# Performance work log

Measured on AMD Instinct MI355X. Metric: run time of the kernel, lower is better.

## Reference

```python
import jax, jax.numpy as jnp
import numpy as np

B, W, H, V, L = 64, 512, 1024, 32000, 2


def setup_inputs() -> dict:
    key = jax.random.key(0)
    ks = jax.random.split(key, 20)
    s = 0.02  # init scale
    n = lambda k, shp: jax.random.normal(k, shp, jnp.float32)
    return {
        "input": jax.random.randint(ks[0], (B, 1), 0, V),
        "h0": n(ks[1], (L, B, H)),
        "c0": n(ks[2], (L, B, H)),
        "encoder_output": n(ks[3], (B, W, H)),
        "embedding": n(ks[4], (V, H)) * s,
        "W_ih0": n(ks[5], (4 * H, H)) * s,
        "W_hh0": n(ks[6], (4 * H, H)) * s,
        "b_ih0": n(ks[7], (4 * H,)) * s,
        "b_hh0": n(ks[8], (4 * H,)) * s,
        "W_ih1": n(ks[9], (4 * H, H)) * s,
        "W_hh1": n(ks[10], (4 * H, H)) * s,
        "b_ih1": n(ks[11], (4 * H,)) * s,
        "b_hh1": n(ks[12], (4 * H,)) * s,
        "att_w": n(ks[13], (2 * H,)) * s,
        "att_b": n(ks[14], (1,)) * s,
        "input_W": n(ks[15], (H, 2 * H)) * s,
        "input_b": n(ks[16], (H,)) * s,
        "out_W": n(ks[17], (V, H)) * s,
        "out_b": n(ks[18], (V,)) * s,
    }


def _lstm_step(x, h, c, W_ih, W_hh, b_ih, b_hh):
    # PyTorch gate order: i, f, g, o
    g = x @ W_ih.T + h @ W_hh.T + b_ih + b_hh
    i, f, gg, o = jnp.split(g, 4, axis=-1)
    c2 = jax.nn.sigmoid(f) * c + jax.nn.sigmoid(i) * jnp.tanh(gg)
    return jax.nn.sigmoid(o) * jnp.tanh(c2), c2


def reference(input, h0, c0, encoder_output, embedding,
              W_ih0, W_hh0, b_ih0, b_hh0, W_ih1, W_hh1, b_ih1, b_hh1,
              att_w, att_b, input_W, input_b, out_W, out_b):
    Hd = h0.shape[-1]
    emb = embedding[input]                       # (B,1,H)
    att_state = h0[-1] * c0[-1]                  # (B,H)
    # Vectorized replacement of the per-word cat+linear loop:
    # att_line(cat(enc_w, att_state)) = enc_w @ w_enc + att_state @ w_st + b
    w_enc, w_st = att_w[:Hd], att_w[Hd:]
    scores = encoder_output @ w_enc + (att_state @ w_st)[:, None] + att_b[0]  # (B,W)
    # Original quirk: weigth starts with a zeros column, then softmax over
    # weigth[:, 0:-1] -> zero column + scores for words 0..W-2 (last dropped).
    zeros = jnp.zeros((scores.shape[0], 1), scores.dtype)
    full = jnp.concatenate([zeros, scores[:, :-1]], axis=1)  # (B,W)
    wts = jax.nn.softmax(full, axis=1)
    ctx = jnp.einsum('bw,bwh->bh', wts, encoder_output)      # (B,H)
    x = jnp.concatenate([ctx, emb[:, 0, :]], axis=-1)        # (B,2H)
    x = x @ input_W.T + input_b                              # (B,H)
    h1, c1 = _lstm_step(x, h0[0], c0[0], W_ih0, W_hh0, b_ih0, b_hh0)
    h2, c2 = _lstm_step(h1, h0[1], c0[1], W_ih1, W_hh1, b_ih1, b_hh1)
    logits = h2 @ out_W.T + out_b                            # (B,V)
    logp = jax.nn.log_softmax(logits, axis=-1)[:, None, :]   # (B,1,V)
    return logp, jnp.stack([h1, h2]), jnp.stack([c1, c2])
```

## Files before the change

kernel.cpp:

```cpp
#include <hip/hip_runtime.h>
#include <hip/hip_bf16.h>

#define Bsz 64
#define Wln 512
#define Hd  1024
#define Vc  32000

typedef short v8s __attribute__((ext_vector_type(8)));
typedef float f32x4 __attribute__((ext_vector_type(4)));

__device__ inline unsigned short f2b(float f) {
  union { float f; unsigned u; } v; v.f = f;
  return (unsigned short)((v.u + 0x8000u) >> 16);
}
__device__ inline float wave_sum(float v) {
  #pragma unroll
  for (int o = 32; o; o >>= 1) v += __shfl_down(v, o);
  return v;
}
__device__ inline float wave_max(float v) {
  #pragma unroll
  for (int o = 32; o; o >>= 1) v = fmaxf(v, __shfl_down(v, o));
  return v;
}
__device__ inline float wave_sum_all(float v) {
  #pragma unroll
  for (int o = 32; o; o >>= 1) v += __shfl_xor(v, o);
  return v;
}
__device__ inline float wave_max_all(float v) {
  #pragma unroll
  for (int o = 32; o; o >>= 1) v = fmaxf(v, __shfl_xor(v, o));
  return v;
}
__device__ inline float sigm(float x) { return 1.f / (1.f + expf(-x)); }

__device__ inline v8s cvt_frag(float4 x0, float4 x1) {
  v8s r;
  r[0] = (short)f2b(x0.x); r[1] = (short)f2b(x0.y);
  r[2] = (short)f2b(x0.z); r[3] = (short)f2b(x0.w);
  r[4] = (short)f2b(x1.x); r[5] = (short)f2b(x1.y);
  r[6] = (short)f2b(x1.z); r[7] = (short)f2b(x1.w);
  return r;
}

__device__ inline void stage_A(const float* __restrict__ A, const float* __restrict__ Ab,
                               int sA, char* pool, int tid) {
  #pragma unroll
  for (int it = 0; it < 16; ++it) {
    int idx = it * 512 + tid;
    int row = idx >> 7, ch = idx & 127;
    const float* src = A + (size_t)row * sA + ch * 8;
    float4 x0 = *(const float4*)src;
    float4 x1 = *(const float4*)(src + 4);
    if (Ab) {
      const float* s2 = Ab + (size_t)row * sA + ch * 8;
      float4 y0 = *(const float4*)s2;
      float4 y1 = *(const float4*)(s2 + 4);
      x0.x += y0.x; x0.y += y0.y; x0.z += y0.z; x0.w += y0.w;
      x1.x += y1.x; x1.y += y1.y; x1.z += y1.z; x1.w += y1.w;
    }
    *(v8s*)(pool + row * 2048 + ((ch * 16) ^ ((row & 7) << 4))) = cvt_frag(x0, x1);
  }
}

__global__ __launch_bounds__(512, 8) void k_attn(
    const float* __restrict__ enc, const float* __restrict__ att_w,
    const float* __restrict__ h0, const float* __restrict__ c0,
    const float* __restrict__ att_b,
    float* __restrict__ ctxp, float* __restrict__ pm_a, float* __restrict__ ps_a)
{
  __shared__ __align__(16) float pool[9 * 1024];
  __shared__ float fullv[8];
  __shared__ float redA[8];
  const int b = blockIdx.x >> 6, ch = blockIdx.x & 63;
  const int c0r = ch * 8;
  const int tid = threadIdx.x, w = tid >> 6, lane = tid & 63;
  const float* encb = enc + (size_t)b * Wln * Hd;

  #pragma unroll
  for (int it = 0; it < 5; ++it) {
    int idx = it * 512 + tid;
    if (idx < 2304) {
      int rl = idx >> 8, c4 = idx & 255;
      int gr = c0r - 1 + rl;
      gr = gr < 0 ? 0 : gr;
      float4 v = *(const float4*)(encb + (size_t)gr * Hd + c4 * 4);
      *(float4*)(pool + rl * 1024 + c4 * 4) = v;
    }
  }

  {
    size_t base = (size_t)(Bsz + b) * Hd;
    int j = tid * 2;
    float s = h0[base + j] * c0[base + j] * att_w[Hd + j]
            + h0[base + j + 1] * c0[base + j + 1] * att_w[Hd + j + 1];
    s = wave_sum(s);
    if (lane == 0) redA[w] = s;
  }
  __syncthreads();
  float sa = att_b[0];
  #pragma unroll
  for (int i = 0; i < 8; ++i) sa += redA[i];

  float4 aw[4];
  #pragma unroll
  for (int s4 = 0; s4 < 4; ++s4)
    aw[s4] = *(const float4*)(att_w + s4 * 256 + lane * 4);

  {
    int j = c0r + w;
    float v = 0.f;
    if (j > 0) {
      const float* rp = pool + w * 1024;
      float s = 0.f;
      #pragma unroll
      for (int s4 = 0; s4 < 4; ++s4) {
        float4 e = *(const float4*)(rp + s4 * 256 + lane * 4);
        s += e.x * aw[s4].x + e.y * aw[s4].y + e.z * aw[s4].z + e.w * aw[s4].w;
      }
      s = wave_sum(s);
      v = s + sa;
    }
    if (lane == 0) fullv[w] = v;
  }
  __syncthreads();

  float mv = (lane < 8) ? fullv[lane] : -1e30f;
  float M = wave_max_all(mv);
  float ev = (lane < 8) ? expf(mv - M) : 0.f;
  float S = wave_sum_all(ev);

  float wt = expf(fullv[w] - M);
  float4 a4[4];
  {
    const float* rp = pool + (w + 1) * 1024;
    #pragma unroll
    for (int s4 = 0; s4 < 4; ++s4) {
      float4 e = *(const float4*)(rp + s4 * 256 + lane * 4);
      a4[s4].x = wt * e.x; a4[s4].y = wt * e.y;
      a4[s4].z = wt * e.z; a4[s4].w = wt * e.w;
    }
  }
  __syncthreads();
  #pragma unroll
  for (int s4 = 0; s4 < 4; ++s4)
    *(float4*)(pool + w * 1024 + s4 * 256 + lane * 4) = a4[s4];
  __syncthreads();

  for (int c = tid; c < Hd; c += 512) {
    float s = 0.f;
    #pragma unroll
    for (int ww = 0; ww < 8; ++ww) s += pool[ww * 1024 + c];
    ctxp[(size_t)(b * 64 + ch) * Hd + c] = s;
  }
  if (tid == 0) { pm_a[b * 64 + ch] = M; ps_a[b * 64 + ch] = S; }
}

__global__ __launch_bounds__(512) void k_ctx_fin(
    const float* __restrict__ ctxp, const float* __restrict__ pm_a,
    const float* __restrict__ ps_a, const int* __restrict__ input,
    const float* __restrict__ emb, float* __restrict__ cat)
{
  __shared__ float scs[64];
  __shared__ float invsh;
  int b = blockIdx.x, tid = threadIdx.x;
  if (tid == 0) {
    float Mg = pm_a[b * 64];
    #pragma unroll
    for (int c = 1; c < 64; ++c) Mg = fmaxf(Mg, pm_a[b * 64 + c]);
    float Sg = 0.f;
    for (int c = 0; c < 64; ++c) {
      float e = expf(pm_a[b * 64 + c] - Mg);
      scs[c] = e;
      Sg += ps_a[b * 64 + c] * e;
    }
    invsh = 1.f / Sg;
  }
  __syncthreads();
  float inv = invsh;
  for (int h = tid; h < Hd; h += 512) {
    float s = 0.f;
    #pragma unroll 8
    for (int c = 0; c < 64; ++c) s += ctxp[(size_t)(b * 64 + c) * Hd + h] * scs[c];
    cat[b * 2 * Hd + h] = s * inv;
  }
  int idx = input[b];
  for (int j = tid; j < Hd; j += 512)
    cat[b * 2 * Hd + Hd + j] = emb[(size_t)idx * Hd + j];
}

__global__ __launch_bounds__(512) void k_input_gemm(
    const float* __restrict__ cat, const float* __restrict__ inW,
    const float* __restrict__ inb, float* __restrict__ x1, float* __restrict__ x2)
{
  __shared__ __align__(16) char pool[131072];
  const int tid = threadIdx.x;
  const int w = tid >> 6, lane = tid & 63;
  const int r = lane & 15, q = lane >> 4;
  const int kh = w;
  const int half = (blockIdx.x >= 64);
  const int n0 = (blockIdx.x & 63) * 16;
  const float* A = cat + half * 1024;
  const float* B = inW + half * 1024;
  float* out = half ? x2 : x1;

  const float* bp = B + (size_t)(n0 + r) * 2048 + kh * 128 + q * 8;
  float4 breg[4][2];
  #pragma unroll
  for (int kk = 0; kk < 4; ++kk) {
    breg[kk][0] = *(const float4*)(bp + kk * 32);
    breg[kk][1] = *(const float4*)(bp + kk * 32 + 4);
  }
  stage_A(A, nullptr, 2048, pool, tid);
  __syncthreads();

  f32x4 acc[4] = {{0,0,0,0},{0,0,0,0},{0,0,0,0},{0,0,0,0}};
  const int swz = (r & 7) << 4;
  #pragma unroll
  for (int kk = 0; kk < 4; ++kk) {
    v8s bf = cvt_frag(breg[kk][0], breg[kk][1]);
    int cb = ((kh * 128 + kk * 32 + q * 8) * 2) ^ swz;
    #pragma unroll
    for (int m = 0; m < 4; ++m) {
      v8s af = *(const v8s*)(pool + (m * 16 + r) * 2048 + cb);
      acc[m] = __builtin_amdgcn_mfma_f32_16x16x32_bf16(af, bf, acc[m], 0, 0, 0);
    }
  }
  __syncthreads();

  float (*red)[64][17] = (float(*)[64][17])pool;
  #pragma unroll
  for (int m = 0; m < 4; ++m)
    #pragma unroll
    for (int rr = 0; rr < 4; ++rr)
      red[w][lane][m * 4 + rr] = acc[m][rr];
  __syncthreads();

  #pragma unroll
  for (int it = 0; it < 2; ++it) {
    int e = it * 512 + tid;
    int cc = e & 15, rowi = e >> 4;
    int idx = ((rowi >> 4) << 2) + (rowi & 3);
    int le  = (((rowi >> 2) & 3) << 4) + cc;
    float s = 0.f;
    #pragma unroll
    for (int j = 0; j < 8; ++j) s += red[j][le][idx];
    float bb = half ? 0.f : inb[n0 + cc];
    out[(size_t)rowi * Hd + n0 + cc] = s + bb;
  }
}

__global__ __launch_bounds__(512) void k_gate_lstm(
    const float* __restrict__ xA, const float* __restrict__ xAb,
    const float* __restrict__ hA,
    const float* __restrict__ W_ih, const float* __restrict__ W_hh,
    const float* __restrict__ b_ih, const float* __restrict__ b_hh,
    const float* __restrict__ c0,
    float* __restrict__ out_h, float* __restrict__ out_c)
{
  __shared__ __align__(16) char pool[131072];
  const int tid = threadIdx.x;
  const int w = tid >> 6, lane = tid & 63;
  const int r = lane & 15, q = lane >> 4;
  const int kh = w;
  const int gate = r >> 2, jl = r & 3;
  const size_t Brow = (size_t)gate * Hd + blockIdx.x * 4 + jl;

  float4 breg[2][4][2];
  {
    const float* bp0 = W_ih + Brow * Hd + kh * 128 + q * 8;
    const float* bp1 = W_hh + Brow * Hd + kh * 128 + q * 8;
    #pragma unroll
    for (int kk = 0; kk < 4; ++kk) {
      breg[0][kk][0] = *(const float4*)(bp0 + kk * 32);
      breg[0][kk][1] = *(const float4*)(bp0 + kk * 32 + 4);
      breg[1][kk][0] = *(const float4*)(bp1 + kk * 32);
      breg[1][kk][1] = *(const float4*)(bp1 + kk * 32 + 4);
    }
  }

  f32x4 acc[4] = {{0,0,0,0},{0,0,0,0},{0,0,0,0},{0,0,0,0}};
  const float* Amat[2] = { xA, hA };
  const float* Abm[2]  = { xAb, nullptr };
  #pragma unroll
  for (int p = 0; p < 2; ++p) {
    stage_A(Amat[p], Abm[p], Hd, pool, tid);
    __syncthreads();
    const int swz = (r & 7) << 4;
    #pragma unroll
    for (int kk = 0; kk < 4; ++kk) {
      v8s bf = cvt_frag(breg[p][kk][0], breg[p][kk][1]);
      int cb = ((kh * 128 + kk * 32 + q * 8) * 2) ^ swz;
      #pragma unroll
      for (int m = 0; m < 4; ++m) {
        v8s af = *(const v8s*)(pool + (m * 16 + r) * 2048 + cb);
        acc[m] = __builtin_amdgcn_mfma_f32_16x16x32_bf16(af, bf, acc[m], 0, 0, 0);
      }
    }
    __syncthreads();
  }

  float (*red)[64][17] = (float(*)[64][17])pool;
  #pragma unroll
  for (int m = 0; m < 4; ++m)
    #pragma unroll
    for (int rr = 0; rr < 4; ++rr)
      red[w][lane][m * 4 + rr] = acc[m][rr];
  __syncthreads();

  if (tid < 256) {
    int b = tid >> 2, jl2 = tid & 3;
    int jg = blockIdx.x * 4 + jl2;
    float gv[4];
    #pragma unroll
    for (int g2 = 0; g2 < 4; ++g2) {
      int cc = g2 * 4 + jl2;
      int idx = ((b >> 4) << 2) + (b & 3);
      int le  = (((b >> 2) & 3) << 4) + cc;
      float s = 0.f;
      #pragma unroll
      for (int j = 0; j < 8; ++j) s += red[j][le][idx];
      gv[g2] = s + b_ih[(size_t)g2 * Hd + jg] + b_hh[(size_t)g2 * Hd + jg];
    }
    float c = sigm(gv[1]) * c0[(size_t)b * Hd + jg] + sigm(gv[0]) * tanhf(gv[2]);
    float h = sigm(gv[3]) * tanhf(c);
    out_h[(size_t)b * Hd + jg] = h;
    out_c[(size_t)b * Hd + jg] = c;
  }
}

__global__ __launch_bounds__(512) void k_logits(
    const float* __restrict__ A, const float* __restrict__ B,
    const float* __restrict__ bias, float* __restrict__ out,
    float* __restrict__ pm, float* __restrict__ ps)
{
  __shared__ __align__(16) char pool[131072];
  const int tid = threadIdx.x;
  const int w = tid >> 6, lane = tid & 63;
  const int r = lane & 15, q = lane >> 4;
  const int nsub = w & 3, kh = w >> 2;
  const int n0 = blockIdx.x * 64;

  const float* bp = B + (size_t)(n0 + nsub * 16 + r) * Hd + kh * 512 + q * 8;
  float4 breg[16][2];
  #pragma unroll
  for (int kk = 0; kk < 16; ++kk) {
    breg[kk][0] = *(const float4*)(bp + kk * 32);
    breg[kk][1] = *(const float4*)(bp + kk * 32 + 4);
  }
  stage_A(A, nullptr, Hd, pool, tid);
  __syncthreads();

  f32x4 acc[4] = {{0,0,0,0},{0,0,0,0},{0,0,0,0},{0,0,0,0}};
  const int swz = (r & 7) << 4;
  #pragma unroll
  for (int kk = 0; kk < 16; ++kk) {
    v8s bf = cvt_frag(breg[kk][0], breg[kk][1]);
    int cb = ((kh * 512 + kk * 32 + q * 8) * 2) ^ swz;
    #pragma unroll
    for (int m = 0; m < 4; ++m) {
      v8s af = *(const v8s*)(pool + (m * 16 + r) * 2048 + cb);
      acc[m] = __builtin_amdgcn_mfma_f32_16x16x32_bf16(af, bf, acc[m], 0, 0, 0);
    }
  }
  __syncthreads();

  float (*red)[64][17] = (float(*)[64][17])pool;
  #pragma unroll
  for (int m = 0; m < 4; ++m)
    #pragma unroll
    for (int rr = 0; rr < 4; ++rr)
      red[w][lane][m * 4 + rr] = acc[m][rr];
  __syncthreads();

  #pragma unroll
  for (int it = 0; it < 8; ++it) {
    int e = it * 512 + tid;
    int cc = e & 63, rowi = e >> 6;
    int ns2 = cc >> 4, lo = cc & 15;
    int idx = ((rowi >> 4) << 2) + (rowi & 3);
    int le  = (((rowi >> 2) & 3) << 4) + lo;
    float val = red[ns2][le][idx] + red[ns2 + 4][le][idx] + bias[n0 + cc];
    out[(size_t)rowi * Vc + n0 + cc] = val;
    float wm = wave_max_all(val);
    float we = wave_sum_all(expf(val - wm));
    if (cc == 0) { pm[blockIdx.x * 64 + rowi] = wm; ps[blockIdx.x * 64 + rowi] = we; }
  }
}

__global__ __launch_bounds__(512) void k_lsm_sub(
    float* __restrict__ lg, const float* __restrict__ pm, const float* __restrict__ ps)
{
  __shared__ float redA[8], redB[8];
  int b = blockIdx.x >> 2, qc = blockIdx.x & 3;
  int tid = threadIdx.x, w = tid >> 6, lane = tid & 63;
  float m = -1e30f;
  for (int j = tid; j < 500; j += 512) m = fmaxf(m, pm[j * 64 + b]);
  m = wave_max(m);
  if (lane == 0) redA[w] = m;
  __syncthreads();
  float M = redA[0];
  #pragma unroll
  for (int i = 1; i < 8; ++i) M = fmaxf(M, redA[i]);
  float s = 0.f;
  for (int j = tid; j < 500; j += 512) s += ps[j * 64 + b] * expf(pm[j * 64 + b] - M);
  s = wave_sum(s);
  if (lane == 0) redB[w] = s;
  __syncthreads();
  float S = redB[0];
  #pragma unroll
  for (int i = 1; i < 8; ++i) S += redB[i];
  float lse = M + logf(S);
  float* row = lg + (size_t)b * Vc + qc * 8000;
  for (int j = tid * 4; j < 8000; j += 2048) {
    float4 v = *(const float4*)(row + j);
    v.x -= lse; v.y -= lse; v.z -= lse; v.w -= lse;
    *(float4*)(row + j) = v;
  }
}

extern "C" void kernel_launch(void* const* d_in, const int* in_sizes, int n_in,
                              void* d_out, int out_size, void* d_ws, size_t ws_size,
                              hipStream_t stream)
{
  const int*   input = (const int*)d_in[0];
  const float* h0    = (const float*)d_in[1];
  const float* c0    = (const float*)d_in[2];
  const float* enc   = (const float*)d_in[3];
  const float* emb   = (const float*)d_in[4];
  const float* W_ih0 = (const float*)d_in[5];
  const float* W_hh0 = (const float*)d_in[6];
  const float* b_ih0 = (const float*)d_in[7];
  const float* b_hh0 = (const float*)d_in[8];
  const float* W_ih1 = (const float*)d_in[9];
  const float* W_hh1 = (const float*)d_in[10];
  const float* b_ih1 = (const float*)d_in[11];
  const float* b_hh1 = (const float*)d_in[12];
  const float* att_w = (const float*)d_in[13];
  const float* att_b = (const float*)d_in[14];
  const float* inW   = (const float*)d_in[15];
  const float* inb   = (const float*)d_in[16];
  const float* outW  = (const float*)d_in[17];
  const float* outb  = (const float*)d_in[18];
  float* out = (float*)d_out;

  char* ws = (char*)d_ws;
  float* cat    = (float*)(ws + 0);
  float* x1     = (float*)(ws + 524288);
  float* x2     = (float*)(ws + 786432);
  float* ctxp   = (float*)(ws + 1048576);
  float* pm_a   = (float*)(ws + 17825792);
  float* ps_a   = (float*)(ws + 17842176);
  float* pm     = (float*)(ws + 17858560);
  float* ps     = (float*)(ws + 17986560);

  float* out_h = out + (size_t)Bsz * Vc;
  float* out_c = out_h + 2 * Bsz * Hd;
  float* h1 = out_h;
  float* h2 = out_h + Bsz * Hd;

  k_attn<<<Bsz * 64, 512, 0, stream>>>(enc, att_w, h0, c0, att_b, ctxp, pm_a, ps_a);
  k_ctx_fin<<<Bsz, 512, 0, stream>>>(ctxp, pm_a, ps_a, input, emb, cat);
  k_input_gemm<<<128, 512, 0, stream>>>(cat, inW, inb, x1, x2);
  k_gate_lstm<<<256, 512, 0, stream>>>(x1, x2, h0, W_ih0, W_hh0, b_ih0, b_hh0,
                                       c0, h1, out_c);
  k_gate_lstm<<<256, 512, 0, stream>>>(h1, nullptr, h0 + (size_t)Bsz * Hd,
                                       W_ih1, W_hh1, b_ih1, b_hh1,
                                       c0 + (size_t)Bsz * Hd, h2, out_c + Bsz * Hd);
  k_logits<<<500, 512, 0, stream>>>(h2, outW, outb, out, pm, ps);
  k_lsm_sub<<<256, 512, 0, stream>>>(out, pm, ps);
}
```

Measured before the change: 149.9 us.

## Drop softmax max-tracking in attention and widen the context-finalize grid

```diff
diff --git a/kernel.cpp b/kernel.cpp
--- a/kernel.cpp
+++ b/kernel.cpp
@@ -64,30 +64,27 @@
   }
 }
 
-__global__ __launch_bounds__(512, 8) void k_attn(
+__global__ __launch_bounds__(512, 4) void k_attn(
     const float* __restrict__ enc, const float* __restrict__ att_w,
     const float* __restrict__ h0, const float* __restrict__ c0,
     const float* __restrict__ att_b,
-    float* __restrict__ ctxp, float* __restrict__ pm_a, float* __restrict__ ps_a)
-{
-  __shared__ __align__(16) float pool[9 * 1024];
-  __shared__ float fullv[8];
+    float* __restrict__ ctxp, float* __restrict__ ps_a)
+{
+  __shared__ __align__(16) float pool[8 * 1024];
+  __shared__ float dots[9];
   __shared__ float redA[8];
+  __shared__ float wts_sh[8];
   const int b = blockIdx.x >> 6, ch = blockIdx.x & 63;
   const int c0r = ch * 8;
   const int tid = threadIdx.x, w = tid >> 6, lane = tid & 63;
   const float* encb = enc + (size_t)b * Wln * Hd;
 
-  #pragma unroll
-  for (int it = 0; it < 5; ++it) {
-    int idx = it * 512 + tid;
-    if (idx < 2304) {
-      int rl = idx >> 8, c4 = idx & 255;
-      int gr = c0r - 1 + rl;
-      gr = gr < 0 ? 0 : gr;
-      float4 v = *(const float4*)(encb + (size_t)gr * Hd + c4 * 4);
-      *(float4*)(pool + rl * 1024 + c4 * 4) = v;
-    }
+  const float* rowp = encb + (size_t)(c0r + w) * Hd;
+  float4 e[4], aw[4];
+  #pragma unroll
+  for (int i = 0; i < 4; ++i) {
+    e[i]  = *(const float4*)(rowp + (i * 64 + lane) * 4);
+    aw[i] = *(const float4*)(att_w + (i * 64 + lane) * 4);
   }
 
   {
@@ -98,54 +95,41 @@
     s = wave_sum(s);
     if (lane == 0) redA[w] = s;
   }
-  __syncthreads();
+
+  {
+    float s = e[0].x*aw[0].x + e[0].y*aw[0].y + e[0].z*aw[0].z + e[0].w*aw[0].w
+            + e[1].x*aw[1].x + e[1].y*aw[1].y + e[1].z*aw[1].z + e[1].w*aw[1].w
+            + e[2].x*aw[2].x + e[2].y*aw[2].y + e[2].z*aw[2].z + e[2].w*aw[2].w
+            + e[3].x*aw[3].x + e[3].y*aw[3].y + e[3].z*aw[3].z + e[3].w*aw[3].w;
+    s = wave_sum(s);
+    if (lane == 0) dots[w + 1] = s;
+  }
+  if (w == 7 && c0r > 0) {
+    const float* hp = encb + (size_t)(c0r - 1) * Hd;
+    float s = 0.f;
+    #pragma unroll
+    for (int i = 0; i < 4; ++i) {
+      float4 hv = *(const float4*)(hp + (i * 64 + lane) * 4);
+      s += hv.x*aw[i].x + hv.y*aw[i].y + hv.z*aw[i].z + hv.w*aw[i].w;
+    }
+    s = wave_sum(s);
+    if (lane == 0) dots[0] = s;
+  }
+  __syncthreads();
+
   float sa = att_b[0];
   #pragma unroll
   for (int i = 0; i < 8; ++i) sa += redA[i];
 
-  float4 aw[4];
-  #pragma unroll
-  for (int s4 = 0; s4 < 4; ++s4)
-    aw[s4] = *(const float4*)(att_w + s4 * 256 + lane * 4);
-
-  {
-    int j = c0r + w;
-    float v = 0.f;
-    if (j > 0) {
-      const float* rp = pool + w * 1024;
-      float s = 0.f;
-      #pragma unroll
-      for (int s4 = 0; s4 < 4; ++s4) {
-        float4 e = *(const float4*)(rp + s4 * 256 + lane * 4);
-        s += e.x * aw[s4].x + e.y * aw[s4].y + e.z * aw[s4].z + e.w * aw[s4].w;
-      }
-      s = wave_sum(s);
-      v = s + sa;
-    }
-    if (lane == 0) fullv[w] = v;
-  }
-  __syncthreads();
-
-  float mv = (lane < 8) ? fullv[lane] : -1e30f;
-  float M = wave_max_all(mv);
-  float ev = (lane < 8) ? expf(mv - M) : 0.f;
-  float S = wave_sum_all(ev);
-
-  float wt = expf(fullv[w] - M);
-  float4 a4[4];
-  {
-    const float* rp = pool + (w + 1) * 1024;
-    #pragma unroll
-    for (int s4 = 0; s4 < 4; ++s4) {
-      float4 e = *(const float4*)(rp + s4 * 256 + lane * 4);
-      a4[s4].x = wt * e.x; a4[s4].y = wt * e.y;
-      a4[s4].z = wt * e.z; a4[s4].w = wt * e.w;
-    }
-  }
-  __syncthreads();
-  #pragma unroll
-  for (int s4 = 0; s4 < 4; ++s4)
-    *(float4*)(pool + w * 1024 + s4 * 256 + lane * 4) = a4[s4];
+  int rw = c0r + w;
+  float wt = (rw == 0) ? 1.f : expf(dots[w] + sa);
+  if (lane == 0) wts_sh[w] = wt;
+
+  #pragma unroll
+  for (int i = 0; i < 4; ++i) {
+    e[i].x *= wt; e[i].y *= wt; e[i].z *= wt; e[i].w *= wt;
+    *(float4*)(pool + w * 1024 + (i * 64 + lane) * 4) = e[i];
+  }
   __syncthreads();
 
   for (int c = tid; c < Hd; c += 512) {
@@ -154,40 +138,32 @@
     for (int ww = 0; ww < 8; ++ww) s += pool[ww * 1024 + c];
     ctxp[(size_t)(b * 64 + ch) * Hd + c] = s;
   }
-  if (tid == 0) { pm_a[b * 64 + ch] = M; ps_a[b * 64 + ch] = S; }
-}
-
-__global__ __launch_bounds__(512) void k_ctx_fin(
-    const float* __restrict__ ctxp, const float* __restrict__ pm_a,
-    const float* __restrict__ ps_a, const int* __restrict__ input,
-    const float* __restrict__ emb, float* __restrict__ cat)
-{
-  __shared__ float scs[64];
-  __shared__ float invsh;
-  int b = blockIdx.x, tid = threadIdx.x;
   if (tid == 0) {
-    float Mg = pm_a[b * 64];
-    #pragma unroll
-    for (int c = 1; c < 64; ++c) Mg = fmaxf(Mg, pm_a[b * 64 + c]);
-    float Sg = 0.f;
-    for (int c = 0; c < 64; ++c) {
-      float e = expf(pm_a[b * 64 + c] - Mg);
-      scs[c] = e;
-      Sg += ps_a[b * 64 + c] * e;
-    }
-    invsh = 1.f / Sg;
-  }
-  __syncthreads();
-  float inv = invsh;
-  for (int h = tid; h < Hd; h += 512) {
-    float s = 0.f;
-    #pragma unroll 8
-    for (int c = 0; c < 64; ++c) s += ctxp[(size_t)(b * 64 + c) * Hd + h] * scs[c];
-    cat[b * 2 * Hd + h] = s * inv;
-  }
+    float S = 0.f;
+    #pragma unroll
+    for (int i = 0; i < 8; ++i) S += wts_sh[i];
+    ps_a[b * 64 + ch] = S;
+  }
+}
+
+__global__ __launch_bounds__(256) void k_ctx_fin(
+    const float* __restrict__ ctxp, const float* __restrict__ ps_a,
+    const int* __restrict__ input, const float* __restrict__ emb,
+    float* __restrict__ cat)
+{
+  int b = blockIdx.x >> 2, qtr = blockIdx.x & 3;
+  int t = threadIdx.x;
+  float S = 0.f;
+  #pragma unroll
+  for (int c = 0; c < 64; ++c) S += ps_a[b * 64 + c];
+  float inv = 1.f / S;
+  int col = qtr * 256 + t;
+  float s = 0.f;
+  #pragma unroll 8
+  for (int c = 0; c < 64; ++c) s += ctxp[(size_t)(b * 64 + c) * Hd + col];
+  cat[b * 2 * Hd + col] = s * inv;
   int idx = input[b];
-  for (int j = tid; j < Hd; j += 512)
-    cat[b * 2 * Hd + Hd + j] = emb[(size_t)idx * Hd + j];
+  cat[b * 2 * Hd + Hd + col] = emb[(size_t)idx * Hd + col];
 }
 
 __global__ __launch_bounds__(512) void k_input_gemm(
@@ -450,18 +426,17 @@
   float* x1     = (float*)(ws + 524288);
   float* x2     = (float*)(ws + 786432);
   float* ctxp   = (float*)(ws + 1048576);
-  float* pm_a   = (float*)(ws + 17825792);
-  float* ps_a   = (float*)(ws + 17842176);
-  float* pm     = (float*)(ws + 17858560);
-  float* ps     = (float*)(ws + 17986560);
+  float* ps_a   = (float*)(ws + 17825792);
+  float* pm     = (float*)(ws + 17842176);
+  float* ps     = (float*)(ws + 17970176);
 
   float* out_h = out + (size_t)Bsz * Vc;
   float* out_c = out_h + 2 * Bsz * Hd;
   float* h1 = out_h;
   float* h2 = out_h + Bsz * Hd;
 
-  k_attn<<<Bsz * 64, 512, 0, stream>>>(enc, att_w, h0, c0, att_b, ctxp, pm_a, ps_a);
-  k_ctx_fin<<<Bsz, 512, 0, stream>>>(ctxp, pm_a, ps_a, input, emb, cat);
+  k_attn<<<Bsz * 64, 512, 0, stream>>>(enc, att_w, h0, c0, att_b, ctxp, ps_a);
+  k_ctx_fin<<<Bsz * 4, 256, 0, stream>>>(ctxp, ps_a, input, emb, cat);
   k_input_gemm<<<128, 512, 0, stream>>>(cat, inW, inb, x1, x2);
   k_gate_lstm<<<256, 512, 0, stream>>>(x1, x2, h0, W_ih0, W_hh0, b_ih0, b_hh0,
                                        c0, h1, out_c);
```

New measurement: 135.5 us. 1.11x faster.
